# Performance work log

Measured on AMD Instinct MI355X. Metric: run time of the kernel, lower is better.

## Reference

```python
import jax, jax.numpy as jnp
import numpy as np


def setup_inputs() -> dict:
    key = jax.random.key(0)
    ks = jax.random.split(key, 6)
    T, B, D, H = 512, 64, 512, 512
    s = 1.0 / np.sqrt(H)  # PyTorch-style uniform-ish scale kept simple as scaled normal
    return {
        "inputs": jax.random.normal(ks[0], (T, B, D), jnp.float32),
        "mask": jnp.ones((T, B), jnp.float32),
        "h0": jax.random.normal(ks[1], (B, H), jnp.float32),
        "W_ih": jax.random.normal(ks[2], (4 * H, D), jnp.float32) * s,
        "W_hh": jax.random.normal(ks[3], (4 * H, H), jnp.float32) * s,
        "b_ih": jax.random.normal(ks[4], (4 * H,), jnp.float32) * s,
        "b_hh": jax.random.normal(ks[5], (4 * H,), jnp.float32) * s,
    }


def _lstm_forward(inputs, mask, h0, c0, W_ih, W_hh, b_ih, b_hh):
    """Masked LSTM over time. inputs [T,B,D], mask [T,B], h0/c0 [B,H].
    Mask blend resets state toward the initial hidden where mask==0,
    exactly as the torch loop does per step."""
    bias = b_ih + b_hh
    # Precompute input projections for all steps: [T,B,4H]
    x_proj = jnp.einsum("tbd,gd->tbg", inputs, W_ih) + bias

    def step(carry, inp):
        h, c = carry
        xg, mt = inp  # xg [B,4H], mt [B]
        gates = xg + h @ W_hh.T
        i, f, g, o = jnp.split(gates, 4, axis=-1)
        i = jax.nn.sigmoid(i)
        f = jax.nn.sigmoid(f)
        g = jnp.tanh(g)
        o = jax.nn.sigmoid(o)
        c_new = f * c + i * g
        h_new = o * jnp.tanh(c_new)
        m = mt[:, None]
        h_new = h_new * m + h0 * (1.0 - m)
        c_new = c_new * m + c0 * (1.0 - m)
        return (h_new, c_new), h_new

    (hT, cT), outs = jax.lax.scan(step, (h0, c0), (x_proj, mask))
    return outs, hT, cT


def reference(inputs, mask, h0, W_ih, W_hh, b_ih, b_hh):
    # torch module uses the SAME random tensor for h0 and c0
    out, hT, cT = _lstm_forward(inputs, mask, h0, h0, W_ih, W_hh, b_ih, b_hh)
    # hidden = (stack over layers) -> [1,B,H] each for single layer
    return out, hT[None], cT[None]
```

## Files before the change

### kernel.cpp

```cpp
#include <hip/hip_runtime.h>
#include <hip/hip_fp16.h>


#define T_DIM 512
#define B_DIM 64
#define D_DIM 512
#define H_DIM 512
#define G_DIM 2048
#define M_DIM (T_DIM * B_DIM)

#define NGROUP 8
#define BPG 32
#define NBLK (NGROUP * BPG)
#define NTHR 512
#define WS 520

typedef __attribute__((ext_vector_type(8))) _Float16 half8;
typedef __attribute__((ext_vector_type(2))) __fp16 fp16x2;
typedef __attribute__((ext_vector_type(4))) float float4v;

#define AT_LD_U(p)    __hip_atomic_load((p), __ATOMIC_RELAXED, __HIP_MEMORY_SCOPE_AGENT)
#define AT_ST_U(p, v) __hip_atomic_store((p), (v), __ATOMIC_RELAXED, __HIP_MEMORY_SCOPE_AGENT)
#define AT_LD_I(p)    __hip_atomic_load((p), __ATOMIC_RELAXED, __HIP_MEMORY_SCOPE_AGENT)
#define AT_ST_I(p, v) __hip_atomic_store((p), (v), __ATOMIC_RELAXED, __HIP_MEMORY_SCOPE_AGENT)
#define AT_LD64(p)    __hip_atomic_load((p), __ATOMIC_RELAXED, __HIP_MEMORY_SCOPE_AGENT)
#define AT_ST64(p, v) __hip_atomic_store((p), (v), __ATOMIC_RELAXED, __HIP_MEMORY_SCOPE_AGENT)

__device__ __forceinline__ float sigf(float x) { return 1.0f / (1.0f + __expf(-x)); }
__device__ __forceinline__ float tanhfast(float x) { return 2.0f / (1.0f + __expf(-2.0f * x)) - 1.0f; }
__device__ __forceinline__ unsigned short f2h(float x) {
  return __builtin_bit_cast(unsigned short, (_Float16)x);
}
__device__ __forceinline__ unsigned pk2h(float a, float b) {
  fp16x2 h = __builtin_amdgcn_cvt_pkrtz(a, b);
  return __builtin_bit_cast(unsigned, h);
}

__global__ __launch_bounds__(256) void xproj_mfma(
    const float* __restrict__ A, const float* __restrict__ W,
    const float* __restrict__ b1, const float* __restrict__ b2,
    __half* __restrict__ C) {
  __shared__ __align__(16) _Float16 As[128 * 72];
  __shared__ __align__(16) _Float16 Bs[128 * 72];
  const int tid = threadIdx.x;
  const int bid = blockIdx.x;
  const int xcd = bid & 7, idx = bid >> 3;
  const int mt = xcd * 32 + (idx >> 4);
  const int nt = idx & 15;
  const int lane = tid & 63;
  const int w = tid >> 6;
  const int wm = w >> 1, wn = w & 1;
  const int fr = lane & 15;
  const int ko = (lane >> 4) * 8;
  const int srow = tid >> 4, sf4 = tid & 15;

  const float* Ab = A + (size_t)(mt * 128) * D_DIM;
  const float* Wb = W + (size_t)(nt * 128) * D_DIM;

  float4v acc[4][4];
#pragma unroll
  for (int m = 0; m < 4; ++m)
#pragma unroll
    for (int n = 0; n < 4; ++n) acc[m][n] = (float4v){0.f, 0.f, 0.f, 0.f};

  for (int k0 = 0; k0 < D_DIM; k0 += 64) {
    float4 aR[8], wR[8];
#pragma unroll
    for (int i = 0; i < 8; ++i) {
      aR[i] = *(const float4*)(Ab + (size_t)(srow + i * 16) * D_DIM + k0 + sf4 * 4);
      wR[i] = *(const float4*)(Wb + (size_t)(srow + i * 16) * D_DIM + k0 + sf4 * 4);
    }
    __syncthreads();
#pragma unroll
    for (int i = 0; i < 8; ++i) {
      int row = srow + i * 16;
      *(uint2*)(As + row * 72 + sf4 * 4) =
          make_uint2(pk2h(aR[i].x, aR[i].y), pk2h(aR[i].z, aR[i].w));
      *(uint2*)(Bs + row * 72 + sf4 * 4) =
          make_uint2(pk2h(wR[i].x, wR[i].y), pk2h(wR[i].z, wR[i].w));
    }
    __syncthreads();
#pragma unroll
    for (int kk = 0; kk < 2; ++kk) {
      half8 af[4], bf[4];
#pragma unroll
      for (int m = 0; m < 4; ++m)
        af[m] = *(const half8*)(As + (wm * 64 + m * 16 + fr) * 72 + kk * 32 + ko);
#pragma unroll
      for (int n = 0; n < 4; ++n)
        bf[n] = *(const half8*)(Bs + (wn * 64 + n * 16 + fr) * 72 + kk * 32 + ko);
#pragma unroll
      for (int m = 0; m < 4; ++m)
#pragma unroll
        for (int n = 0; n < 4; ++n)
          acc[m][n] = __builtin_amdgcn_mfma_f32_16x16x32_f16(af[m], bf[n], acc[m][n], 0, 0, 0);
    }
  }
#pragma unroll
  for (int n = 0; n < 4; ++n) {
    int gcol = nt * 128 + wn * 64 + n * 16 + fr;
    float bias = b1[gcol] + b2[gcol];
#pragma unroll
    for (int m = 0; m < 4; ++m) {
      size_t grow = (size_t)(mt * 128 + wm * 64 + m * 16 + (lane >> 4) * 4);
      __half* cp = C + grow * G_DIM + gcol;
#pragma unroll
      for (int r = 0; r < 4; ++r)
        cp[(size_t)r * G_DIM] = (__half)(acc[m][n][r] + bias);
    }
  }
}

__global__ __launch_bounds__(NTHR) void lstm_seq(
    const __half* __restrict__ xproj, const float* __restrict__ mask,
    const float* __restrict__ h0, const float* __restrict__ Whh,
    float* __restrict__ out, unsigned short* __restrict__ hbuf,
    int* slot_base) {
  extern __shared__ char smemc[];
  unsigned short* Wl = (unsigned short*)smemc;
  unsigned short* hl = Wl + 64 * WS;
  float* part = (float*)(hl + 16 * WS);

  const int tid = threadIdx.x;
  const int blk = blockIdx.x;
  const int grp = blk & 7;
  const int rank = blk >> 3;
  const int bbase = grp * 8;
  const int jbase = rank * 16;
  int* slots = (int*)((char*)slot_base + grp * 128);

  for (int idx = tid; idx < 64 * 128; idx += NTHR) {
    int r = idx >> 7;
    int k4 = (idx & 127) << 2;
    int grow = (r >> 4) * H_DIM + jbase + (r & 15);
    float4 wv = *(const float4*)(Whh + (size_t)grow * H_DIM + k4);
    *(uint2*)(Wl + r * WS + k4) = make_uint2(pk2h(wv.x, wv.y), pk2h(wv.z, wv.w));
  }

  const int eb = tid >> 4, ejl = tid & 15;
  const int bglob = bbase + eb;
  const int jglob = jbase + ejl;
  float h0v = 0.0f, cval = 0.0f;
  float xpv0 = 0.f, xpv1 = 0.f, xpv2 = 0.f, xpv3 = 0.f, mval = 1.f;
  if (tid < 128) {
    h0v = h0[bglob * H_DIM + jglob];
    cval = h0v;
  }

  {
    int mybits = (tid < 128) ? (int)f2h(h0v) : 0;
    int nb1 = __shfl_down(mybits, 1, 64);
    int nb2 = __shfl_down(mybits, 2, 64);
    int nb3 = __shfl_down(mybits, 3, 64);
    if (tid < 128 && ((ejl & 3) == 0)) {
      unsigned lo = (unsigned)mybits | ((unsigned)nb1 << 16);
      unsigned hi = (unsigned)nb2 | ((unsigned)nb3 << 16);
      AT_ST64((unsigned long long*)hbuf + bglob * 128 + (jglob >> 2),
              ((unsigned long long)hi << 32) | lo);
    }
  }
  __syncthreads();
  if (tid == 0) AT_ST_I(&slots[rank], 1);
  if (tid < 128) {
    mval = mask[bglob];
    const __half* xb = xproj + (size_t)bglob * G_DIM + jglob;
    xpv0 = (float)xb[0];
    xpv1 = (float)xb[512];
    xpv2 = (float)xb[1024];
    xpv3 = (float)xb[1536];
  }
  if (tid < 64) {
    int v;
    do {
      v = (tid < BPG) ? AT_LD_I(&slots[tid]) : 1;
      if (__all(v >= 1)) break;
      __builtin_amdgcn_s_sleep(2);
    } while (true);
  }
  __syncthreads();
  __asm__ volatile("" ::: "memory");

  const int w = tid >> 6;
  const int lane = tid & 63;
  const int q = w & 3;
  const int ks = w >> 2;
  const int am = lane & 15;
  const int koct = (lane >> 4) * 8;
  const int br = q * 16 + (lane & 15);

  for (int ts = 0; ts < T_DIM; ++ts) {
    const unsigned long long* cur64 =
        (const unsigned long long*)hbuf + (ts & 1) * (B_DIM * H_DIM / 4) +
        (size_t)bbase * 128;
    unsigned long long* nxt64 =
        (unsigned long long*)hbuf + ((ts + 1) & 1) * (B_DIM * H_DIM / 4);

#pragma unroll
    for (int i = 0; i < 2; ++i) {
      int v = tid + i * NTHR;
      unsigned long long u = AT_LD64(cur64 + v);
      ((unsigned long long*)hl)[(v >> 7) * 130 + (v & 127)] = u;
    }
    __syncthreads();

    float4v acc = {0.f, 0.f, 0.f, 0.f};
#pragma unroll
    for (int kc = 0; kc < 8; ++kc) {
      int k = ks * 256 + kc * 32 + koct;
      half8 a = *(const half8*)((const _Float16*)hl + am * WS + k);
      half8 b8 = *(const half8*)((const _Float16*)Wl + br * WS + k);
      acc = __builtin_amdgcn_mfma_f32_16x16x32_f16(a, b8, acc, 0, 0, 0);
    }
#pragma unroll
    for (int reg = 0; reg < 4; ++reg) {
      int m = (lane >> 4) * 4 + reg;
      part[w * 256 + m * 16 + (lane & 15)] = acc[reg];
    }
    __syncthreads();

    float hnew = 0.f;
    if (tid < 128) {
      int o = eb * 16 + ejl;
      float iv = sigf(part[0 * 256 + o] + part[4 * 256 + o] + xpv0);
      float fv = sigf(part[1 * 256 + o] + part[5 * 256 + o] + xpv1);
      float gv = tanhfast(part[2 * 256 + o] + part[6 * 256 + o] + xpv2);
      float ov = sigf(part[3 * 256 + o] + part[7 * 256 + o] + xpv3);
      float cn = fv * cval + iv * gv;
      float hn = ov * tanhfast(cn);
      hnew = hn * mval + h0v * (1.0f - mval);
      cval = cn * mval + h0v * (1.0f - mval);
    }
    {
      int mybits = (tid < 128) ? (int)f2h(hnew) : 0;
      int nb1 = __shfl_down(mybits, 1, 64);
      int nb2 = __shfl_down(mybits, 2, 64);
      int nb3 = __shfl_down(mybits, 3, 64);
      if (tid < 128 && ((ejl & 3) == 0)) {
        unsigned lo = (unsigned)mybits | ((unsigned)nb1 << 16);
        unsigned hi = (unsigned)nb2 | ((unsigned)nb3 << 16);
        AT_ST64(nxt64 + bglob * 128 + (jglob >> 2),
                ((unsigned long long)hi << 32) | lo);
      }
    }
    __syncthreads();
    if (tid == 0) AT_ST_I(&slots[rank], ts + 2);

    if (tid < 128) {
      out[((size_t)ts * B_DIM + bglob) * H_DIM + jglob] = hnew;
      if (ts == T_DIM - 1) {
        out[(size_t)T_DIM * B_DIM * H_DIM + bglob * H_DIM + jglob] = hnew;
        out[(size_t)T_DIM * B_DIM * H_DIM + B_DIM * H_DIM + bglob * H_DIM + jglob] = cval;
      } else {
        mval = mask[(ts + 1) * B_DIM + bglob];
        const __half* xb = xproj + ((size_t)(ts + 1) * B_DIM + bglob) * G_DIM + jglob;
        xpv0 = (float)xb[0];
        xpv1 = (float)xb[512];
        xpv2 = (float)xb[1024];
        xpv3 = (float)xb[1536];
      }
    }

    if (tid < 64) {
      int v;
      do {
        v = (tid < BPG) ? AT_LD_I(&slots[tid]) : (ts + 2);
        if (__all(v >= ts + 2)) break;
        __builtin_amdgcn_s_sleep(2);
      } while (true);
    }
    __syncthreads();
    __asm__ volatile("" ::: "memory");
  }
}

extern "C" void kernel_launch(void* const* d_in, const int* in_sizes, int n_in,
                              void* d_out, int out_size, void* d_ws, size_t ws_size,
                              hipStream_t stream) {
  const float* inputs = (const float*)d_in[0];
  const float* maskp  = (const float*)d_in[1];
  const float* h0     = (const float*)d_in[2];
  const float* W_ih   = (const float*)d_in[3];
  const float* W_hh   = (const float*)d_in[4];
  const float* b_ih   = (const float*)d_in[5];
  const float* b_hh   = (const float*)d_in[6];
  float* out = (float*)d_out;

  char* ws = (char*)d_ws;
  int* slot_base = (int*)ws;
  unsigned short* hbuf = (unsigned short*)(ws + 4096);
  __half* xp = (__half*)(ws + 4096 + 2 * (size_t)B_DIM * H_DIM * sizeof(unsigned short));

  (void)hipMemsetAsync(d_ws, 0, 4096, stream);

  size_t ldsB = (size_t)(64 * WS * 2 + 16 * WS * 2 + 2048 * 4);

  xproj_mfma<<<dim3((M_DIM / 128) * (G_DIM / 128)), 256, 0, stream>>>(
      inputs, W_ih, b_ih, b_hh, xp);
  lstm_seq<<<NBLK, NTHR, ldsB, stream>>>(xp, maskp, h0, W_hh, out, hbuf, slot_base);

  (void)in_sizes; (void)n_in; (void)out_size; (void)ws_size;
}
```

Measured before the change: 1.489 ms.

## Fuse input projection into recurrent LSTM kernel using LDS-resident W_ih slice

Removes the separate xproj GEMM kernel and its fp16 intermediate buffer. Each persistent block now keeps its W_ih slice in LDS next to W_hh and computes the next step's input projection with MFMA after publishing h, intending to overlap it with the cross-block wait. This removes a kernel launch and the large xproj write/read, but adds input loads and MFMA work, plus an extra barrier, inside the latency-bound per-step loop. LDS use per block roughly doubles.

```diff
diff --git a/kernel.cpp b/kernel.cpp
--- a/kernel.cpp
+++ b/kernel.cpp
@@ -6,7 +6,6 @@
 #define B_DIM 64
 #define D_DIM 512
 #define H_DIM 512
-#define G_DIM 2048
 #define M_DIM (T_DIM * B_DIM)
 
 #define NGROUP 8
@@ -19,8 +18,6 @@
 typedef __attribute__((ext_vector_type(2))) __fp16 fp16x2;
 typedef __attribute__((ext_vector_type(4))) float float4v;
 
-#define AT_LD_U(p)    __hip_atomic_load((p), __ATOMIC_RELAXED, __HIP_MEMORY_SCOPE_AGENT)
-#define AT_ST_U(p, v) __hip_atomic_store((p), (v), __ATOMIC_RELAXED, __HIP_MEMORY_SCOPE_AGENT)
 #define AT_LD_I(p)    __hip_atomic_load((p), __ATOMIC_RELAXED, __HIP_MEMORY_SCOPE_AGENT)
 #define AT_ST_I(p, v) __hip_atomic_store((p), (v), __ATOMIC_RELAXED, __HIP_MEMORY_SCOPE_AGENT)
 #define AT_LD64(p)    __hip_atomic_load((p), __ATOMIC_RELAXED, __HIP_MEMORY_SCOPE_AGENT)
@@ -36,89 +33,17 @@
   return __builtin_bit_cast(unsigned, h);
 }
 
-__global__ __launch_bounds__(256) void xproj_mfma(
-    const float* __restrict__ A, const float* __restrict__ W,
-    const float* __restrict__ b1, const float* __restrict__ b2,
-    __half* __restrict__ C) {
-  __shared__ __align__(16) _Float16 As[128 * 72];
-  __shared__ __align__(16) _Float16 Bs[128 * 72];
-  const int tid = threadIdx.x;
-  const int bid = blockIdx.x;
-  const int xcd = bid & 7, idx = bid >> 3;
-  const int mt = xcd * 32 + (idx >> 4);
-  const int nt = idx & 15;
-  const int lane = tid & 63;
-  const int w = tid >> 6;
-  const int wm = w >> 1, wn = w & 1;
-  const int fr = lane & 15;
-  const int ko = (lane >> 4) * 8;
-  const int srow = tid >> 4, sf4 = tid & 15;
-
-  const float* Ab = A + (size_t)(mt * 128) * D_DIM;
-  const float* Wb = W + (size_t)(nt * 128) * D_DIM;
-
-  float4v acc[4][4];
-#pragma unroll
-  for (int m = 0; m < 4; ++m)
-#pragma unroll
-    for (int n = 0; n < 4; ++n) acc[m][n] = (float4v){0.f, 0.f, 0.f, 0.f};
-
-  for (int k0 = 0; k0 < D_DIM; k0 += 64) {
-    float4 aR[8], wR[8];
-#pragma unroll
-    for (int i = 0; i < 8; ++i) {
-      aR[i] = *(const float4*)(Ab + (size_t)(srow + i * 16) * D_DIM + k0 + sf4 * 4);
-      wR[i] = *(const float4*)(Wb + (size_t)(srow + i * 16) * D_DIM + k0 + sf4 * 4);
-    }
-    __syncthreads();
-#pragma unroll
-    for (int i = 0; i < 8; ++i) {
-      int row = srow + i * 16;
-      *(uint2*)(As + row * 72 + sf4 * 4) =
-          make_uint2(pk2h(aR[i].x, aR[i].y), pk2h(aR[i].z, aR[i].w));
-      *(uint2*)(Bs + row * 72 + sf4 * 4) =
-          make_uint2(pk2h(wR[i].x, wR[i].y), pk2h(wR[i].z, wR[i].w));
-    }
-    __syncthreads();
-#pragma unroll
-    for (int kk = 0; kk < 2; ++kk) {
-      half8 af[4], bf[4];
-#pragma unroll
-      for (int m = 0; m < 4; ++m)
-        af[m] = *(const half8*)(As + (wm * 64 + m * 16 + fr) * 72 + kk * 32 + ko);
-#pragma unroll
-      for (int n = 0; n < 4; ++n)
-        bf[n] = *(const half8*)(Bs + (wn * 64 + n * 16 + fr) * 72 + kk * 32 + ko);
-#pragma unroll
-      for (int m = 0; m < 4; ++m)
-#pragma unroll
-        for (int n = 0; n < 4; ++n)
-          acc[m][n] = __builtin_amdgcn_mfma_f32_16x16x32_f16(af[m], bf[n], acc[m][n], 0, 0, 0);
-    }
-  }
-#pragma unroll
-  for (int n = 0; n < 4; ++n) {
-    int gcol = nt * 128 + wn * 64 + n * 16 + fr;
-    float bias = b1[gcol] + b2[gcol];
-#pragma unroll
-    for (int m = 0; m < 4; ++m) {
-      size_t grow = (size_t)(mt * 128 + wm * 64 + m * 16 + (lane >> 4) * 4);
-      __half* cp = C + grow * G_DIM + gcol;
-#pragma unroll
-      for (int r = 0; r < 4; ++r)
-        cp[(size_t)r * G_DIM] = (__half)(acc[m][n][r] + bias);
-    }
-  }
-}
-
 __global__ __launch_bounds__(NTHR) void lstm_seq(
-    const __half* __restrict__ xproj, const float* __restrict__ mask,
+    const float* __restrict__ inputs, const float* __restrict__ mask,
     const float* __restrict__ h0, const float* __restrict__ Whh,
+    const float* __restrict__ Wih, const float* __restrict__ b_ih,
+    const float* __restrict__ b_hh,
     float* __restrict__ out, unsigned short* __restrict__ hbuf,
     int* slot_base) {
   extern __shared__ char smemc[];
   unsigned short* Wl = (unsigned short*)smemc;
-  unsigned short* hl = Wl + 64 * WS;
+  unsigned short* Xw = Wl + 64 * WS;
+  unsigned short* hl = Xw + 64 * WS;
   float* part = (float*)(hl + 16 * WS);
 
   const int tid = threadIdx.x;
@@ -135,16 +60,22 @@
     int grow = (r >> 4) * H_DIM + jbase + (r & 15);
     float4 wv = *(const float4*)(Whh + (size_t)grow * H_DIM + k4);
     *(uint2*)(Wl + r * WS + k4) = make_uint2(pk2h(wv.x, wv.y), pk2h(wv.z, wv.w));
+    float4 xv = *(const float4*)(Wih + (size_t)grow * D_DIM + k4);
+    *(uint2*)(Xw + r * WS + k4) = make_uint2(pk2h(xv.x, xv.y), pk2h(xv.z, xv.w));
   }
 
   const int eb = tid >> 4, ejl = tid & 15;
   const int bglob = bbase + eb;
   const int jglob = jbase + ejl;
-  float h0v = 0.0f, cval = 0.0f;
-  float xpv0 = 0.f, xpv1 = 0.f, xpv2 = 0.f, xpv3 = 0.f, mval = 1.f;
+  float h0v = 0.0f, cval = 0.0f, mval = 1.f;
+  float bi_ = 0.f, bf_ = 0.f, bg_ = 0.f, bo_ = 0.f;
   if (tid < 128) {
     h0v = h0[bglob * H_DIM + jglob];
     cval = h0v;
+    bi_ = b_ih[0 * H_DIM + jglob] + b_hh[0 * H_DIM + jglob];
+    bf_ = b_ih[1 * H_DIM + jglob] + b_hh[1 * H_DIM + jglob];
+    bg_ = b_ih[2 * H_DIM + jglob] + b_hh[2 * H_DIM + jglob];
+    bo_ = b_ih[3 * H_DIM + jglob] + b_hh[3 * H_DIM + jglob];
   }
 
   {
@@ -161,13 +92,35 @@
   }
   __syncthreads();
   if (tid == 0) AT_ST_I(&slots[rank], 1);
-  if (tid < 128) {
-    mval = mask[bglob];
-    const __half* xb = xproj + (size_t)bglob * G_DIM + jglob;
-    xpv0 = (float)xb[0];
-    xpv1 = (float)xb[512];
-    xpv2 = (float)xb[1024];
-    xpv3 = (float)xb[1536];
+  if (tid < 128) mval = mask[bglob];
+
+  const int w = tid >> 6;
+  const int lane = tid & 63;
+  const int q = w & 3;
+  const int ks = w >> 2;
+  const int am = lane & 15;
+  const int koct = (lane >> 4) * 8;
+  const int br = q * 16 + (lane & 15);
+
+  float4v xacc = {0.f, 0.f, 0.f, 0.f};
+  {
+    const float* xin = inputs + (size_t)bbase * D_DIM;
+#pragma unroll
+    for (int i = 0; i < 4; ++i) {
+      int idx = tid + i * NTHR;
+      int r = idx >> 8;
+      int cl = idx & 255;
+      float2 xv = *(const float2*)(xin + (size_t)r * D_DIM + cl * 2);
+      ((unsigned*)hl)[r * (WS / 2) + cl] = pk2h(xv.x, xv.y);
+    }
+    __syncthreads();
+#pragma unroll
+    for (int kc = 0; kc < 8; ++kc) {
+      int k = ks * 256 + kc * 32 + koct;
+      half8 a = *(const half8*)((const _Float16*)hl + am * WS + k);
+      half8 b8 = *(const half8*)((const _Float16*)Xw + br * WS + k);
+      xacc = __builtin_amdgcn_mfma_f32_16x16x32_f16(a, b8, xacc, 0, 0, 0);
+    }
   }
   if (tid < 64) {
     int v;
@@ -180,14 +133,6 @@
   __syncthreads();
   __asm__ volatile("" ::: "memory");
 
-  const int w = tid >> 6;
-  const int lane = tid & 63;
-  const int q = w & 3;
-  const int ks = w >> 2;
-  const int am = lane & 15;
-  const int koct = (lane >> 4) * 8;
-  const int br = q * 16 + (lane & 15);
-
   for (int ts = 0; ts < T_DIM; ++ts) {
     const unsigned long long* cur64 =
         (const unsigned long long*)hbuf + (ts & 1) * (B_DIM * H_DIM / 4) +
@@ -203,7 +148,7 @@
     }
     __syncthreads();
 
-    float4v acc = {0.f, 0.f, 0.f, 0.f};
+    float4v acc = xacc;
 #pragma unroll
     for (int kc = 0; kc < 8; ++kc) {
       int k = ks * 256 + kc * 32 + koct;
@@ -221,10 +166,10 @@
     float hnew = 0.f;
     if (tid < 128) {
       int o = eb * 16 + ejl;
-      float iv = sigf(part[0 * 256 + o] + part[4 * 256 + o] + xpv0);
-      float fv = sigf(part[1 * 256 + o] + part[5 * 256 + o] + xpv1);
-      float gv = tanhfast(part[2 * 256 + o] + part[6 * 256 + o] + xpv2);
-      float ov = sigf(part[3 * 256 + o] + part[7 * 256 + o] + xpv3);
+      float iv = sigf(part[0 * 256 + o] + part[4 * 256 + o] + bi_);
+      float fv = sigf(part[1 * 256 + o] + part[5 * 256 + o] + bf_);
+      float gv = tanhfast(part[2 * 256 + o] + part[6 * 256 + o] + bg_);
+      float ov = sigf(part[3 * 256 + o] + part[7 * 256 + o] + bo_);
       float cn = fv * cval + iv * gv;
       float hn = ov * tanhfast(cn);
       hnew = hn * mval + h0v * (1.0f - mval);
@@ -245,19 +190,34 @@
     __syncthreads();
     if (tid == 0) AT_ST_I(&slots[rank], ts + 2);
 
-    if (tid < 128) {
+    if (ts + 1 < T_DIM) {
+      const float* xin = inputs + ((size_t)(ts + 1) * B_DIM + bbase) * D_DIM;
+#pragma unroll
+      for (int i = 0; i < 4; ++i) {
+        int idx = tid + i * NTHR;
+        int r = idx >> 8;
+        int cl = idx & 255;
+        float2 xv = *(const float2*)(xin + (size_t)r * D_DIM + cl * 2);
+        ((unsigned*)hl)[r * (WS / 2) + cl] = pk2h(xv.x, xv.y);
+      }
+      __syncthreads();
+      if (tid < 128) {
+        out[((size_t)ts * B_DIM + bglob) * H_DIM + jglob] = hnew;
+        mval = mask[(ts + 1) * B_DIM + bglob];
+      }
+      float4v xa = {0.f, 0.f, 0.f, 0.f};
+#pragma unroll
+      for (int kc = 0; kc < 8; ++kc) {
+        int k = ks * 256 + kc * 32 + koct;
+        half8 a = *(const half8*)((const _Float16*)hl + am * WS + k);
+        half8 b8 = *(const half8*)((const _Float16*)Xw + br * WS + k);
+        xa = __builtin_amdgcn_mfma_f32_16x16x32_f16(a, b8, xa, 0, 0, 0);
+      }
+      xacc = xa;
+    } else if (tid < 128) {
       out[((size_t)ts * B_DIM + bglob) * H_DIM + jglob] = hnew;
-      if (ts == T_DIM - 1) {
-        out[(size_t)T_DIM * B_DIM * H_DIM + bglob * H_DIM + jglob] = hnew;
-        out[(size_t)T_DIM * B_DIM * H_DIM + B_DIM * H_DIM + bglob * H_DIM + jglob] = cval;
-      } else {
-        mval = mask[(ts + 1) * B_DIM + bglob];
-        const __half* xb = xproj + ((size_t)(ts + 1) * B_DIM + bglob) * G_DIM + jglob;
-        xpv0 = (float)xb[0];
-        xpv1 = (float)xb[512];
-        xpv2 = (float)xb[1024];
-        xpv3 = (float)xb[1536];
-      }
+      out[(size_t)T_DIM * B_DIM * H_DIM + bglob * H_DIM + jglob] = hnew;
+      out[(size_t)T_DIM * B_DIM * H_DIM + B_DIM * H_DIM + bglob * H_DIM + jglob] = cval;
     }
 
     if (tid < 64) {
@@ -288,15 +248,13 @@
   char* ws = (char*)d_ws;
   int* slot_base = (int*)ws;
   unsigned short* hbuf = (unsigned short*)(ws + 4096);
-  __half* xp = (__half*)(ws + 4096 + 2 * (size_t)B_DIM * H_DIM * sizeof(unsigned short));
 
   (void)hipMemsetAsync(d_ws, 0, 4096, stream);
 
-  size_t ldsB = (size_t)(64 * WS * 2 + 16 * WS * 2 + 2048 * 4);
-
-  xproj_mfma<<<dim3((M_DIM / 128) * (G_DIM / 128)), 256, 0, stream>>>(
-      inputs, W_ih, b_ih, b_hh, xp);
-  lstm_seq<<<NBLK, NTHR, ldsB, stream>>>(xp, maskp, h0, W_hh, out, hbuf, slot_base);
+  size_t ldsB = (size_t)(64 * WS * 2 * 2 + 16 * WS * 2 + 2048 * 4);
+
+  lstm_seq<<<NBLK, NTHR, ldsB, stream>>>(inputs, maskp, h0, W_hh, W_ih, b_ih, b_hh,
+                                         out, hbuf, slot_base);
 
   (void)in_sizes; (void)n_in; (void)out_size; (void)ws_size;
 }
```

Result: slower. 1.658 ms (+11.3%).
